# Optimization experiments

Hardware: AMD Instinct MI355X
Metric: run time of the kernel (lower is better)

Reference implementation:

```python
import jax, jax.numpy as jnp
import numpy as np

EPS = 1e-6
H, KV, HD = 16, 4, 64      # q heads, kv heads, head dim
BLK = 32                   # dllm_block_length (block-diffusion attention)
TOPK = 2                   # experts per token

def rmsnorm(x, w):
    return x * jax.lax.rsqrt(jnp.mean(x * x, axis=-1, keepdims=True) + EPS) * w

def rotate_half(x):
    x1, x2 = jnp.split(x, 2, axis=-1)
    return jnp.concatenate([-x2, x1], axis=-1)

def setup_inputs() -> dict:
    key = jax.random.key(0)
    ks = jax.random.split(key, 12)
    B, S, D = 1, 2048, 1024
    E, I = 8, 1024
    s = 0.02
    pos = jnp.arange(S, dtype=jnp.float32)
    inv_freq = 1.0 / (10000.0 ** (jnp.arange(0, HD, 2, dtype=jnp.float32) / HD))
    emb = jnp.concatenate([jnp.outer(pos, inv_freq)] * 2, axis=-1)  # [S, HD]
    return {
        'hidden_states': jax.random.normal(ks[0], (B, S, D), jnp.float32),
        'cos': jnp.cos(emb), 'sin': jnp.sin(emb),
        'w_qkv': jax.random.normal(ks[1], (D, (H + 2 * KV) * HD), jnp.float32) * s,
        'w_o': jax.random.normal(ks[2], (H * HD, D), jnp.float32) * s,
        'q_norm_w': jnp.ones((HD,), jnp.float32),
        'k_norm_w': jnp.ones((HD,), jnp.float32),
        'in_ln_w': jnp.ones((D,), jnp.float32),
        'post_ln_w': jnp.ones((D,), jnp.float32),
        'router_w': jax.random.normal(ks[3], (D, E), jnp.float32) * s,
        'w_gate': jax.random.normal(ks[4], (E, D, I), jnp.float32) * s,
        'w_up': jax.random.normal(ks[5], (E, D, I), jnp.float32) * s,
        'w_down': jax.random.normal(ks[6], (E, I, D), jnp.float32) * s,
        'ws_gate': jax.random.normal(ks[7], (D, I), jnp.float32) * s,
        'ws_up': jax.random.normal(ks[8], (D, I), jnp.float32) * s,
        'ws_down': jax.random.normal(ks[9], (I, D), jnp.float32) * s,
    }

def reference(hidden_states, cos, sin, w_qkv, w_o, q_norm_w, k_norm_w, in_ln_w,
              post_ln_w, router_w, w_gate, w_up, w_down, ws_gate, ws_up, ws_down):
    B, S, D = hidden_states.shape
    scale = HD ** -0.5
    # --- attention (pre-norm) ---
    h = rmsnorm(hidden_states, in_ln_w)
    qkv = h @ w_qkv
    q, k, v = jnp.split(qkv, [H * HD, (H + KV) * HD], axis=-1)
    q = q.reshape(B, S, H, HD); k = k.reshape(B, S, KV, HD); v = v.reshape(B, S, KV, HD)
    q = rmsnorm(q, q_norm_w); k = rmsnorm(k, k_norm_w)   # qk-norm per head
    c = cos[None, :, None, :]; sn = sin[None, :, None, :]
    q = q * c + rotate_half(q) * sn
    k = k * c + rotate_half(k) * sn
    rep = H // KV
    k = jnp.repeat(k, rep, axis=2); v = jnp.repeat(v, rep, axis=2)  # GQA expand
    scores = jnp.einsum('bqhd,bkhd->bhqk', q, k) * scale
    blk = jnp.arange(S) // BLK
    mask = blk[:, None] >= blk[None, :]   # block-causal: full attn inside block
    scores = jnp.where(mask[None, None], scores, jnp.float32(-1e30))
    p = jax.nn.softmax(scores, axis=-1)
    attn = jnp.einsum('bhqk,bkhd->bqhd', p, v).reshape(B, S, H * HD)
    x = hidden_states + attn @ w_o
    # --- MoE FFN (pre-norm) ---
    h2 = rmsnorm(x, post_ln_w)
    t = h2.reshape(B * S, D)
    logits = t.astype(jnp.float32) @ router_w.astype(jnp.float32)  # fp32 router
    probs = jax.nn.softmax(logits, axis=-1)
    topv, topi = jax.lax.top_k(probs, TOPK)
    topv = topv / jnp.sum(topv, axis=-1, keepdims=True)            # norm_topk_prob
    E = router_w.shape[1]
    w_tok = jnp.zeros((t.shape[0], E), jnp.float32).at[
        jnp.arange(t.shape[0])[:, None], topi].set(topv).astype(t.dtype)
    g = jnp.einsum('td,edi->tei', t, w_gate)
    u = jnp.einsum('td,edi->tei', t, w_up)
    eo = jnp.einsum('tei,eid->ted', jax.nn.silu(g) * u, w_down)
    moe = jnp.einsum('te,ted->td', w_tok, eo)
    shared = (jax.nn.silu(t @ ws_gate) * (t @ ws_up)) @ ws_down
    return x + (moe + shared).reshape(B, S, D)
```

## Files before the change

### kernel.cpp

```cpp
#include <hip/hip_runtime.h>
#include <hip/hip_bf16.h>
#include <math.h>

#define S 2048
#define D 1024
#define NH 16
#define NKV 4
#define HD 64
#define QKV_N 1536
#define NE 8
#define NI 1024
#define EPS 1e-6f

typedef __bf16 bf16_t;
typedef __bf16 __attribute__((may_alias)) abf16;
typedef __attribute__((ext_vector_type(8))) __bf16 bf16x8;
typedef __attribute__((ext_vector_type(4))) float f32x4;
union I4B8 { int4 i; bf16x8 v; bf16_t e[8]; };

__device__ __forceinline__ void gll16(const void* g, void* l) {
  __builtin_amdgcn_global_load_lds(
      (const __attribute__((address_space(1))) void*)g,
      (__attribute__((address_space(3))) void*)l, 16, 0, 0);
}


__global__ void rmsnorm_kernel(const float* __restrict__ in, const float* __restrict__ w,
                               float* __restrict__ out32, __hip_bfloat16* __restrict__ out16) {
  int t = blockIdx.x;
  int tid = threadIdx.x;
  const float* row = in + (size_t)t * D;
  float v[4];
  float ss = 0.f;
#pragma unroll
  for (int i = 0; i < 4; ++i) {
    v[i] = row[tid + i * 256];
    ss += v[i] * v[i];
  }
#pragma unroll
  for (int off = 32; off; off >>= 1) ss += __shfl_xor(ss, off);
  __shared__ float wsum[4];
  int wave = tid >> 6;
  if ((tid & 63) == 0) wsum[wave] = ss;
  __syncthreads();
  float tot = wsum[0] + wsum[1] + wsum[2] + wsum[3];
  float r = rsqrtf(tot / (float)D + EPS);
#pragma unroll
  for (int i = 0; i < 4; ++i) {
    int d = tid + i * 256;
    float val = v[i] * r * w[d];
    if (out32) out32[(size_t)t * D + d] = val;
    if (out16) out16[(size_t)t * D + d] = __float2bfloat16(val);
  }
}

__global__ void rmsnorm_router_kernel(const float* __restrict__ in, const float* __restrict__ w,
                                      const float* __restrict__ rw,
                                      __hip_bfloat16* __restrict__ out16,
                                      int* __restrict__ topk_e, float* __restrict__ topk_w) {
  int t = blockIdx.x;
  int tid = threadIdx.x;
  const float* row = in + (size_t)t * D;
  float v[4];
  float ss = 0.f;
#pragma unroll
  for (int i = 0; i < 4; ++i) {
    v[i] = row[tid + i * 256];
    ss += v[i] * v[i];
  }
#pragma unroll
  for (int off = 32; off; off >>= 1) ss += __shfl_xor(ss, off);
  __shared__ float wsum[4];
  __shared__ float pl[4][NE];
  int wave = tid >> 6, lane = tid & 63;
  if (lane == 0) wsum[wave] = ss;
  __syncthreads();
  float tot = wsum[0] + wsum[1] + wsum[2] + wsum[3];
  float r = rsqrtf(tot / (float)D + EPS);
  float p[NE] = {};
#pragma unroll
  for (int i = 0; i < 4; ++i) {
    int d = tid + i * 256;
    float val = v[i] * r * w[d];
    out16[(size_t)t * D + d] = __float2bfloat16(val);
    const float* rwd = rw + (size_t)d * NE;
#pragma unroll
    for (int e = 0; e < NE; ++e) p[e] += val * rwd[e];
  }
#pragma unroll
  for (int off = 32; off; off >>= 1)
#pragma unroll
    for (int e = 0; e < NE; ++e) p[e] += __shfl_xor(p[e], off);
  if (lane == 0)
#pragma unroll
    for (int e = 0; e < NE; ++e) pl[wave][e] = p[e];
  __syncthreads();
  if (tid == 0) {
    float q[NE];
#pragma unroll
    for (int e = 0; e < NE; ++e) q[e] = pl[0][e] + pl[1][e] + pl[2][e] + pl[3][e];
    float mx = q[0];
#pragma unroll
    for (int e = 1; e < NE; ++e) mx = fmaxf(mx, q[e]);
    float ex[NE];
#pragma unroll
    for (int e = 0; e < NE; ++e) ex[e] = __expf(q[e] - mx);
    int e0 = 0;
#pragma unroll
    for (int e = 1; e < NE; ++e) if (ex[e] > ex[e0]) e0 = e;
    int e1 = (e0 == 0) ? 1 : 0;
#pragma unroll
    for (int e = 0; e < NE; ++e) if (e != e0 && ex[e] > ex[e1]) e1 = e;
    float w0 = ex[e0] / (ex[e0] + ex[e1]);
    float w1 = ex[e1] / (ex[e0] + ex[e1]);
    topk_e[2 * t] = e0;  topk_e[2 * t + 1] = e1;
    topk_w[2 * t] = w0;  topk_w[2 * t + 1] = w1;
  }
}

__global__ void transpose_all_kernel(
    const float* __restrict__ w_qkv, const float* __restrict__ w_o,
    const float* __restrict__ w_gate, const float* __restrict__ w_up,
    const float* __restrict__ w_down, const float* __restrict__ ws_gate,
    const float* __restrict__ ws_up, const float* __restrict__ ws_down,
    __hip_bfloat16* wqkvT, __hip_bfloat16* woT, __hip_bfloat16* wgT,
    __hip_bfloat16* wuT, __hip_bfloat16* wdT, __hip_bfloat16* wsgT,
    __hip_bfloat16* wsuT, __hip_bfloat16* wsdT,
    const float* __restrict__ hidden, const float* __restrict__ in_ln,
    __hip_bfloat16* __restrict__ hb_out) {
  int z = blockIdx.z;
  int tid = threadIdx.x;
  if (z == 29) {
    __shared__ float wsum[4];
    int base = ((int)blockIdx.y * 24 + (int)blockIdx.x) * 6;
    int wave = tid >> 6;
#pragma unroll
    for (int jj = 0; jj < 6; ++jj) {
      int t = base + jj;
      if (t < S) {
        const float* row = hidden + (size_t)t * D;
        float v[4];
        float ss = 0.f;
#pragma unroll
        for (int i = 0; i < 4; ++i) {
          v[i] = row[tid + i * 256];
          ss += v[i] * v[i];
        }
#pragma unroll
        for (int off = 32; off; off >>= 1) ss += __shfl_xor(ss, off);
        if ((tid & 63) == 0) wsum[wave] = ss;
        __syncthreads();
        float tot = wsum[0] + wsum[1] + wsum[2] + wsum[3];
        float r = rsqrtf(tot / (float)D + EPS);
#pragma unroll
        for (int i = 0; i < 4; ++i) {
          int d = tid + i * 256;
          hb_out[(size_t)t * D + d] = __float2bfloat16(v[i] * r * in_ln[d]);
        }
      }
      __syncthreads();
    }
    return;
  }
  __shared__ __align__(16) bf16_t tile[64][72];
  const float* W; __hip_bfloat16* WT; int Kd, Nd;
  if (z == 0)       { W = w_qkv;  WT = wqkvT; Kd = D;  Nd = QKV_N; }
  else if (z == 1)  { W = w_o;    WT = woT;   Kd = D;  Nd = D; }
  else if (z < 10)  { int e = z - 2;  W = w_gate + (size_t)e * D * NI; WT = wgT + (size_t)e * D * NI; Kd = D;  Nd = NI; }
  else if (z < 18)  { int e = z - 10; W = w_up   + (size_t)e * D * NI; WT = wuT + (size_t)e * D * NI; Kd = D;  Nd = NI; }
  else if (z < 26)  { int e = z - 18; W = w_down + (size_t)e * NI * D; WT = wdT + (size_t)e * NI * D; Kd = NI; Nd = D; }
  else if (z == 26) { W = ws_gate; WT = wsgT; Kd = D;  Nd = NI; }
  else if (z == 27) { W = ws_up;   WT = wsuT; Kd = D;  Nd = NI; }
  else              { W = ws_down; WT = wsdT; Kd = NI; Nd = D; }
  int n0 = blockIdx.x * 64, k0 = blockIdx.y * 64;
  if (n0 >= Nd || k0 >= Kd) return;
  int rk = tid >> 4;
  int rc = (tid & 15) * 4;
#pragma unroll
  for (int it = 0; it < 4; ++it) {
    int k = it * 16 + rk;
    float4 v = *(const float4*)(W + (size_t)(k0 + k) * Nd + n0 + rc);
    union { bf16_t e[4]; int2 q; } pk4;
    pk4.e[0] = (bf16_t)v.x; pk4.e[1] = (bf16_t)v.y;
    pk4.e[2] = (bf16_t)v.z; pk4.e[3] = (bf16_t)v.w;
    *(int2*)&tile[k][rc] = pk4.q;
  }
  __syncthreads();
  int n = tid >> 2;
  int kc = (tid & 3) * 16;
  union { bf16_t e[16]; int4 q[2]; } pk;
#pragma unroll
  for (int j = 0; j < 16; ++j) pk.e[j] = tile[kc + j][n];
  int4* outp = (int4*)(WT + (size_t)(n0 + n) * Kd + k0 + kc);
  outp[0] = pk.q[0];
  outp[1] = pk.q[1];
}

__global__ __launch_bounds__(256) void mgemm_kernel(
    const __hip_bfloat16* __restrict__ A, const __hip_bfloat16* __restrict__ BT,
    const float* __restrict__ Cadd, float* __restrict__ C,
    int M, int N, int K,
    const int* __restrict__ counts, const int* __restrict__ offsets,
    const int* __restrict__ tok, int a_comp,
    const __hip_bfloat16* __restrict__ As2, const __hip_bfloat16* __restrict__ BTs2,
    float* __restrict__ Cs2) {
  __shared__ __align__(16) bf16_t Asd[2][128 * 32];
  __shared__ __align__(16) bf16_t Bsd[2][128 * 32];
  __shared__ int rowmap[128];
  int e = blockIdx.z;
  bool sh = (counts != nullptr) && (e == NE);
  int cnt = sh ? M : (counts ? counts[e] : M);
  int bm = blockIdx.y * 128;
  if (bm >= cnt) return;
  int bn = blockIdx.x * 128;
  int obase = sh ? 0 : (offsets ? offsets[e] : 0);
  const bf16_t* Ab = sh ? (const bf16_t*)As2 : (const bf16_t*)A;
  const bf16_t* BTe = sh ? (const bf16_t*)BTs2 : ((const bf16_t*)BT + (size_t)e * N * K);
  float* Cp = sh ? Cs2 : C;
  const int* toke = (!sh && tok) ? tok + e * S : nullptr;
  int acompe = sh ? 0 : a_comp;
  int tid = threadIdx.x;
  if (tid < 128) {
    int gp = bm + tid;
    int cp = gp < cnt ? gp : cnt - 1;
    rowmap[tid] = toke ? toke[cp] : (acompe ? obase + cp : cp);
  }
  __syncthreads();
  int wave = tid >> 6, lane = tid & 63;
  int quad = lane >> 4, l16 = lane & 15;
  int wm = wave >> 1, wn = wave & 1;
  int srow = tid >> 2, scol = (tid & 3) * 8;
  size_t aoff0 = (size_t)rowmap[srow] * K + scol;
  size_t aoff1 = (size_t)rowmap[64 + srow] * K + scol;
  size_t boff0 = (size_t)(bn + srow) * K + scol;
  size_t boff1 = (size_t)(bn + 64 + srow) * K + scol;
  f32x4 acc[4][4];
#pragma unroll
  for (int i = 0; i < 4; ++i)
#pragma unroll
    for (int j = 0; j < 4; ++j) acc[i][j] = (f32x4){0.f, 0.f, 0.f, 0.f};

  {
    char* AsB = (char*)Asd[0] + wave * 1024;
    char* BsB = (char*)Bsd[0] + wave * 1024;
    gll16(Ab + aoff0, AsB);
    gll16(Ab + aoff1, AsB + 4096);
    gll16(BTe + boff0, BsB);
    gll16(BTe + boff1, BsB + 4096);
  }
  for (int k0 = 0; k0 < K; k0 += 32) {
    int cur = (k0 >> 5) & 1;
    __syncthreads();
    if (k0 + 32 < K) {
      char* AsB = (char*)Asd[cur ^ 1] + wave * 1024;
      char* BsB = (char*)Bsd[cur ^ 1] + wave * 1024;
      gll16(Ab + aoff0 + k0 + 32, AsB);
      gll16(Ab + aoff1 + k0 + 32, AsB + 4096);
      gll16(BTe + boff0 + k0 + 32, BsB);
      gll16(BTe + boff1 + k0 + 32, BsB + 4096);
    }
    I4B8 af[4], bfr[4];
#pragma unroll
    for (int i = 0; i < 4; ++i)
      af[i].i = *(const int4*)(Asd[cur] + (wm * 64 + i * 16 + l16) * 32 + quad * 8);
#pragma unroll
    for (int j = 0; j < 4; ++j)
      bfr[j].i = *(const int4*)(Bsd[cur] + (wn * 64 + j * 16 + l16) * 32 + quad * 8);
#pragma unroll
    for (int i = 0; i < 4; ++i)
#pragma unroll
      for (int j = 0; j < 4; ++j)
        acc[i][j] = __builtin_amdgcn_mfma_f32_16x16x32_bf16(af[i].v, bfr[j].v, acc[i][j], 0, 0, 0);
  }
#pragma unroll
  for (int i = 0; i < 4; ++i) {
#pragma unroll
    for (int r = 0; r < 4; ++r) {
      int trow = wm * 64 + i * 16 + quad * 4 + r;
      int gp = bm + trow;
      if (gp < cnt) {
        size_t rowb = (size_t)(obase + gp) * N;
#pragma unroll
        for (int j = 0; j < 4; ++j) {
          int col = bn + wn * 64 + j * 16 + l16;
          size_t idx = rowb + col;
          Cp[idx] = acc[i][j][r] + (Cadd ? Cadd[idx] : 0.f);
        }
      }
    }
  }
}

__global__ __launch_bounds__(256) void mgemm_gu_kernel(
    const __hip_bfloat16* __restrict__ A, const __hip_bfloat16* __restrict__ BTg,
    const __hip_bfloat16* __restrict__ BTu, __hip_bfloat16* __restrict__ act,
    int M, int N, int K,
    const int* __restrict__ counts, const int* __restrict__ offsets,
    const int* __restrict__ tok,
    const __hip_bfloat16* __restrict__ BTgs, const __hip_bfloat16* __restrict__ BTus,
    __hip_bfloat16* __restrict__ acts) {
  __shared__ __align__(16) bf16_t Asd[2][128 * 32];
  __shared__ __align__(16) bf16_t Bgd[2][64 * 32];
  __shared__ __align__(16) bf16_t Bud[2][64 * 32];
  __shared__ int rowmap[128];
  int e = blockIdx.z;
  bool sh = (counts != nullptr) && (e == NE);
  int cnt = sh ? M : (counts ? counts[e] : M);
  int bm = blockIdx.y * 128;
  if (bm >= cnt) return;
  int bn = blockIdx.x * 64;
  const bf16_t* Ab = (const bf16_t*)A;
  const bf16_t* Bg = sh ? (const bf16_t*)BTgs : ((const bf16_t*)BTg + (size_t)e * N * K);
  const bf16_t* Bu = sh ? (const bf16_t*)BTus : ((const bf16_t*)BTu + (size_t)e * N * K);
  bf16_t* outp = sh ? (bf16_t*)acts : (bf16_t*)act;
  int obase = sh ? 0 : (offsets ? offsets[e] : 0);
  const int* toke = (!sh && tok) ? tok + e * S : nullptr;
  int tid = threadIdx.x;
  if (tid < 128) {
    int gp = bm + tid;
    int cp = gp < cnt ? gp : cnt - 1;
    rowmap[tid] = toke ? toke[cp] : cp;
  }
  __syncthreads();
  int wave = tid >> 6, lane = tid & 63;
  int quad = lane >> 4, l16 = lane & 15;
  int wm = wave >> 1, wn = wave & 1;
  int srow = tid >> 2, scol = (tid & 3) * 8;
  size_t aoff0 = (size_t)rowmap[srow] * K + scol;
  size_t aoff1 = (size_t)rowmap[64 + srow] * K + scol;
  size_t boff = (size_t)(bn + srow) * K + scol;
  f32x4 accg[4][2], accu[4][2];
#pragma unroll
  for (int i = 0; i < 4; ++i)
#pragma unroll
    for (int j = 0; j < 2; ++j) {
      accg[i][j] = (f32x4){0.f, 0.f, 0.f, 0.f};
      accu[i][j] = (f32x4){0.f, 0.f, 0.f, 0.f};
    }
  {
    char* AsB = (char*)Asd[0] + wave * 1024;
    gll16(Ab + aoff0, AsB);
    gll16(Ab + aoff1, AsB + 4096);
    gll16(Bg + boff, (char*)Bgd[0] + wave * 1024);
    gll16(Bu + boff, (char*)Bud[0] + wave * 1024);
  }
  for (int k0 = 0; k0 < K; k0 += 32) {
    int cur = (k0 >> 5) & 1;
    __syncthreads();
    if (k0 + 32 < K) {
      char* AsB = (char*)Asd[cur ^ 1] + wave * 1024;
      gll16(Ab + aoff0 + k0 + 32, AsB);
      gll16(Ab + aoff1 + k0 + 32, AsB + 4096);
      gll16(Bg + boff + k0 + 32, (char*)Bgd[cur ^ 1] + wave * 1024);
      gll16(Bu + boff + k0 + 32, (char*)Bud[cur ^ 1] + wave * 1024);
    }
    I4B8 af[4], bg[2], bu[2];
#pragma unroll
    for (int i = 0; i < 4; ++i)
      af[i].i = *(const int4*)(Asd[cur] + (wm * 64 + i * 16 + l16) * 32 + quad * 8);
#pragma unroll
    for (int j = 0; j < 2; ++j) {
      bg[j].i = *(const int4*)(Bgd[cur] + (wn * 32 + j * 16 + l16) * 32 + quad * 8);
      bu[j].i = *(const int4*)(Bud[cur] + (wn * 32 + j * 16 + l16) * 32 + quad * 8);
    }
#pragma unroll
    for (int i = 0; i < 4; ++i)
#pragma unroll
      for (int j = 0; j < 2; ++j) {
        accg[i][j] = __builtin_amdgcn_mfma_f32_16x16x32_bf16(af[i].v, bg[j].v, accg[i][j], 0, 0, 0);
        accu[i][j] = __builtin_amdgcn_mfma_f32_16x16x32_bf16(af[i].v, bu[j].v, accu[i][j], 0, 0, 0);
      }
  }
#pragma unroll
  for (int i = 0; i < 4; ++i) {
#pragma unroll
    for (int r = 0; r < 4; ++r) {
      int trow = wm * 64 + i * 16 + quad * 4 + r;
      int gp = bm + trow;
      if (gp < cnt) {
        size_t rowb = (size_t)(obase + gp) * N;
#pragma unroll
        for (int j = 0; j < 2; ++j) {
          int col = bn + wn * 32 + j * 16 + l16;
          float g = accg[i][j][r], uu = accu[i][j][r];
          float sg = g / (1.f + __expf(-g));
          outp[rowb + col] = __float2bfloat16(sg * uu);
        }
      }
    }
  }
}

__global__ void qkv_post_kernel(const float* __restrict__ qkv,
                                const float* __restrict__ qw, const float* __restrict__ kw,
                                const float* __restrict__ cosb, const float* __restrict__ sinb,
                                __hip_bfloat16* __restrict__ qout,
                                __hip_bfloat16* __restrict__ kout,
                                __hip_bfloat16* __restrict__ vT) {
  __shared__ float tile[32][33];
  if (blockIdx.y == 5) {
    int bx = blockIdx.x;
    if (bx < 512) {
      int t0 = (bx & 63) * 32;
      int c0 = (bx >> 6) * 32;
      int tx = threadIdx.x & 31, ty = threadIdx.x >> 5;
#pragma unroll
      for (int i = 0; i < 4; ++i)
        tile[ty + i * 8][tx] = qkv[(size_t)(t0 + ty + i * 8) * QKV_N + (NH + NKV) * HD + c0 + tx];
      __syncthreads();
#pragma unroll
      for (int i = 0; i < 4; ++i)
        vT[(size_t)(c0 + ty + i * 8) * S + t0 + tx] = __float2bfloat16(tile[tx][ty + i * 8]);
    }
    return;
  }
  int t = blockIdx.x;
  int u = blockIdx.y * 4 + (threadIdx.x >> 6);
  int lane = threadIdx.x & 63;
  bool isq = (u < NH);
  int h = isq ? u : (u - NH);
  size_t src = (size_t)t * QKV_N + (isq ? (h * HD) : (NH * HD + h * HD)) + lane;
  float xv = qkv[src];
  float ss = xv * xv;
#pragma unroll
  for (int off = 32; off; off >>= 1) ss += __shfl_xor(ss, off);
  float r = rsqrtf(ss * (1.f / 64.f) + EPS);
  float xn = xv * r * (isq ? qw[lane] : kw[lane]);
  float other = __shfl_xor(xn, 32);
  float rot = (lane < 32) ? -other : other;
  float res = xn * cosb[t * 64 + lane] + rot * sinb[t * 64 + lane];
  if (isq) qout[(size_t)t * (NH * HD) + h * HD + lane] = __float2bfloat16(res * 0.125f);
  else     kout[(size_t)t * (NKV * HD) + h * HD + lane] = __float2bfloat16(res);
}

__global__ __launch_bounds__(256) void attn_kernel(
    const __hip_bfloat16* __restrict__ qg, const __hip_bfloat16* __restrict__ kg,
    const __hip_bfloat16* __restrict__ vT,
    float* __restrict__ opart0, float* __restrict__ opart1,
    float* __restrict__ mpart, float* __restrict__ lpart) {
  int qt = (int)(gridDim.x - 1) - (int)blockIdx.x;
  int kvh = blockIdx.y;
  int z = blockIdx.z;
  int tid = threadIdx.x;
  int wave = tid >> 6, lane = tid & 63;
  int quad = lane >> 4, l16 = lane & 15;
  int h = kvh * 4 + wave;

  float* opz = z ? opart1 : opart0;
  float* mp = mpart + (size_t)z * S * NH;
  float* lp = lpart + (size_t)z * S * NH;

  int nb = (qt >> 1) + 1;
  int nt = (nb + 1) >> 1;
  bool halfm = (nb & 1) != 0;
  int h0 = nt >> 1;
  int lo = z ? h0 : 0;
  int hi = z ? nt : h0;

  if (lo >= hi) {
    int row = qt * 16 + (tid >> 4);
    float* od = opz + (size_t)row * (NH * HD) + kvh * 256 + (tid & 15) * 16;
    int4 zz = {0, 0, 0, 0};
#pragma unroll
    for (int i = 0; i < 4; ++i) *(int4*)(od + i * 4) = zz;
    if (tid < 64) {
      int rr = qt * 16 + (tid >> 2), hh = kvh * 4 + (tid & 3);
      mp[(size_t)rr * NH + hh] = -1e30f;
      lp[(size_t)rr * NH + hh] = 0.f;
    }
    return;
  }

  __shared__ __align__(16) int KsI[64 * 36];
  __shared__ __align__(16) int VTI[64 * 36];
  __shared__ __align__(16) int PsI[4][16 * 36];

  I4B8 qf[2];
#pragma unroll
  for (int ch = 0; ch < 2; ++ch)
    qf[ch].i = *(const int4*)((const abf16*)qg +
        (size_t)(qt * 16 + l16) * (NH * HD) + h * HD + ch * 32 + quad * 8);

  I4B8 ones;
  ones.i = (int4){0x3F803F80, 0x3F803F80, 0x3F803F80, 0x3F803F80};

  float m_r[4];
  f32x4 o[4], o4;
#pragma unroll
  for (int r = 0; r < 4; ++r) m_r[r] = -1e30f;
#pragma unroll
  for (int sub = 0; sub < 4; ++sub) o[sub] = (f32x4){0.f, 0.f, 0.f, 0.f};
  o4 = (f32x4){0.f, 0.f, 0.f, 0.f};

  int sp = tid >> 3, sc = tid & 7;
  const abf16* kb = (const abf16*)kg;
  const abf16* vb = (const abf16*)vT;

  int4 rk0 = *(const int4*)(kb + (size_t)(lo * 64 + sp) * (NKV * HD) + kvh * HD + sc * 8);
  int4 rk1 = *(const int4*)(kb + (size_t)(lo * 64 + 32 + sp) * (NKV * HD) + kvh * HD + sc * 8);
  int4 rv0 = *(const int4*)(vb + (size_t)(kvh * HD + sp) * S + lo * 64 + sc * 8);
  int4 rv1 = *(const int4*)(vb + (size_t)(kvh * HD + 32 + sp) * S + lo * 64 + sc * 8);

  for (int kc = lo; kc < hi; ++kc) {
    *(int4*)&KsI[sp * 36 + sc * 4] = rk0;
    *(int4*)&KsI[(sp + 32) * 36 + sc * 4] = rk1;
    *(int4*)&VTI[sp * 36 + sc * 4] = rv0;
    *(int4*)&VTI[(sp + 32) * 36 + sc * 4] = rv1;
    __syncthreads();

    if (kc + 1 < hi) {
      rk0 = *(const int4*)(kb + (size_t)((kc + 1) * 64 + sp) * (NKV * HD) + kvh * HD + sc * 8);
      rk1 = *(const int4*)(kb + (size_t)((kc + 1) * 64 + 32 + sp) * (NKV * HD) + kvh * HD + sc * 8);
      rv0 = *(const int4*)(vb + (size_t)(kvh * HD + sp) * S + (kc + 1) * 64 + sc * 8);
      rv1 = *(const int4*)(vb + (size_t)(kvh * HD + 32 + sp) * S + (kc + 1) * 64 + sc * 8);
    }

    f32x4 s[4];
#pragma unroll
    for (int sub = 0; sub < 4; ++sub) s[sub] = (f32x4){0.f, 0.f, 0.f, 0.f};
    __builtin_amdgcn_s_setprio(1);
#pragma unroll
    for (int sub = 0; sub < 4; ++sub)
#pragma unroll
      for (int ch = 0; ch < 2; ++ch) {
        I4B8 ku;
        ku.i = *(const int4*)&KsI[(sub * 16 + l16) * 36 + ch * 16 + quad * 4];
        s[sub] = __builtin_amdgcn_mfma_f32_16x16x32_bf16(qf[ch].v, ku.v, s[sub], 0, 0, 0);
      }
    __builtin_amdgcn_s_setprio(0);
    if (halfm && kc == nt - 1) {
#pragma unroll
      for (int r = 0; r < 4; ++r) { s[2][r] = -1e30f; s[3][r] = -1e30f; }
    }

    abf16* pw = (abf16*)PsI[wave];
#pragma unroll
    for (int r = 0; r < 4; ++r) {
      float v = fmaxf(fmaxf(s[0][r], s[1][r]), fmaxf(s[2][r], s[3][r]));
#pragma unroll
      for (int off = 1; off < 16; off <<= 1) v = fmaxf(v, __shfl_xor(v, off));
      float mx = fmaxf(m_r[r], v);
      float al = __expf(m_r[r] - mx);
      m_r[r] = mx;
      float p0 = __expf(s[0][r] - mx);
      float p1 = __expf(s[1][r] - mx);
      float p2 = __expf(s[2][r] - mx);
      float p3 = __expf(s[3][r] - mx);
      int prow = quad * 4 + r;
      pw[prow * 72 + l16]      = (bf16_t)p0;
      pw[prow * 72 + 16 + l16] = (bf16_t)p1;
      pw[prow * 72 + 32 + l16] = (bf16_t)p2;
      pw[prow * 72 + 48 + l16] = (bf16_t)p3;
      o4[r] *= al;
#pragma unroll
      for (int sub = 0; sub < 4; ++sub) o[sub][r] *= al;
    }

    I4B8 pu[2];
#pragma unroll
    for (int ch = 0; ch < 2; ++ch)
      pu[ch].i = *(const int4*)&PsI[wave][l16 * 36 + ch * 16 + quad * 4];
    __builtin_amdgcn_s_setprio(1);
#pragma unroll
    for (int sub = 0; sub < 4; ++sub)
#pragma unroll
      for (int ch = 0; ch < 2; ++ch) {
        I4B8 vf;
        vf.i = *(const int4*)&VTI[(sub * 16 + l16) * 36 + ch * 16 + quad * 4];
        o[sub] = __builtin_amdgcn_mfma_f32_16x16x32_bf16(pu[ch].v, vf.v, o[sub], 0, 0, 0);
      }
#pragma unroll
    for (int ch = 0; ch < 2; ++ch)
      o4 = __builtin_amdgcn_mfma_f32_16x16x32_bf16(pu[ch].v, ones.v, o4, 0, 0, 0);
    __builtin_amdgcn_s_setprio(0);
    __syncthreads();
  }

#pragma unroll
  for (int r = 0; r < 4; ++r) {
    int row = qt * 16 + quad * 4 + r;
    float* od = opz + (size_t)row * (NH * HD) + h * HD;
#pragma unroll
    for (int sub = 0; sub < 4; ++sub)
      od[sub * 16 + l16] = o[sub][r];
    if (l16 == 0) {
      mp[(size_t)row * NH + h] = m_r[r];
      lp[(size_t)row * NH + h] = o4[r];
    }
  }
}

__global__ void attn_merge_kernel(const float* __restrict__ opart0,
                                  const float* __restrict__ opart1,
                                  const float* __restrict__ mpart,
                                  const float* __restrict__ lpart,
                                  __hip_bfloat16* __restrict__ attn) {
  int row = blockIdx.x;
  int tid = threadIdx.x;
#pragma unroll
  for (int i = 0; i < 4; ++i) {
    int c = tid + i * 256;
    int h = c >> 6;
    float m0 = mpart[(size_t)row * NH + h];
    float m1 = mpart[(size_t)(S + row) * NH + h];
    float l0 = lpart[(size_t)row * NH + h];
    float l1 = lpart[(size_t)(S + row) * NH + h];
    float M = fmaxf(m0, m1);
    float a0 = __expf(m0 - M), a1 = __expf(m1 - M);
    float l = l0 * a0 + l1 * a1;
    float v = (opart0[(size_t)row * (NH * HD) + c] * a0 +
               opart1[(size_t)row * (NH * HD) + c] * a1) / l;
    attn[(size_t)row * (NH * HD) + c] = __float2bfloat16(v);
  }
}

__global__ __launch_bounds__(1024) void router_place_kernel(
    const int* __restrict__ topk_e, int* __restrict__ counts, int* __restrict__ offsets,
    int* __restrict__ tok_list, int* __restrict__ topk_pos) {
  __shared__ int lcnt[NE];
  int tid = threadIdx.x;
  int lane = tid & 63;
  if (tid < NE) lcnt[tid] = 0;
  __syncthreads();
#pragma unroll
  for (int r = 0; r < 2; ++r) {
    int t = r * 1024 + tid;
#pragma unroll
    for (int s = 0; s < 2; ++s) {
      int e = topk_e[2 * t + s];
      int pos = 0;
#pragma unroll
      for (int x = 0; x < NE; ++x) {
        unsigned long long mask = __ballot(e == x);
        if (mask) {
          int leader = __ffsll((unsigned long long)mask) - 1;
          int cnt = __popcll(mask);
          int base = 0;
          if (lane == leader) base = atomicAdd(&lcnt[x], cnt);
          base = __shfl(base, leader);
          if (e == x)
            pos = base + __popcll(mask & ((1ull << lane) - 1ull));
        }
      }
      topk_pos[2 * t + s] = pos;
      tok_list[e * S + pos] = t;
    }
  }
  __syncthreads();
  if (tid == 0) {
    int acc = 0;
    for (int e = 0; e < NE; ++e) { offsets[e] = acc; counts[e] = lcnt[e]; acc += lcnt[e]; }
  }
}

__global__ void final_kernel(const float* __restrict__ x, const float* __restrict__ sout,
                             const float* __restrict__ eo,
                             const int* __restrict__ topk_e, const int* __restrict__ topk_pos,
                             const float* __restrict__ topk_w, const int* __restrict__ offsets,
                             float* __restrict__ out) {
  int t = blockIdx.x;
  int tid = threadIdx.x;
  int e0 = topk_e[2 * t], e1 = topk_e[2 * t + 1];
  size_t r0 = (size_t)offsets[e0] + topk_pos[2 * t];
  size_t r1 = (size_t)offsets[e1] + topk_pos[2 * t + 1];
  float w0 = topk_w[2 * t], w1 = topk_w[2 * t + 1];
#pragma unroll
  for (int i = 0; i < 4; ++i) {
    int d = tid + i * 256;
    size_t idx = (size_t)t * D + d;
    out[idx] = x[idx] + sout[idx] + w0 * eo[r0 * D + d] + w1 * eo[r1 * D + d];
  }
}

extern "C" void kernel_launch(void* const* d_in, const int* in_sizes, int n_in,
                              void* d_out, int out_size, void* d_ws, size_t ws_size,
                              hipStream_t stream) {
  const float* hidden  = (const float*)d_in[0];
  const float* cosb    = (const float*)d_in[1];
  const float* sinb    = (const float*)d_in[2];
  const float* w_qkv   = (const float*)d_in[3];
  const float* w_o     = (const float*)d_in[4];
  const float* q_norm  = (const float*)d_in[5];
  const float* k_norm  = (const float*)d_in[6];
  const float* in_ln   = (const float*)d_in[7];
  const float* post_ln = (const float*)d_in[8];
  const float* router_w= (const float*)d_in[9];
  const float* w_gate  = (const float*)d_in[10];
  const float* w_up    = (const float*)d_in[11];
  const float* w_down  = (const float*)d_in[12];
  const float* ws_gate = (const float*)d_in[13];
  const float* ws_up   = (const float*)d_in[14];
  const float* ws_down = (const float*)d_in[15];
  float* out = (float*)d_out;
  float* ws = (float*)d_ws;

  typedef __hip_bfloat16 hbf;
  hbf* wqkvT = (hbf*)(ws);
  hbf* woT   = (hbf*)(ws +  768 * 1024);
  hbf* wgT   = (hbf*)(ws + 1280 * 1024);
  hbf* wuT   = (hbf*)(ws + 5376 * 1024);
  hbf* wdT   = (hbf*)(ws + 9472 * 1024);
  hbf* wsgT  = (hbf*)(ws + 13568 * 1024);
  hbf* wsuT  = (hbf*)(ws + 14080 * 1024);
  hbf* wsdT  = (hbf*)(ws + 14592 * 1024);
  hbf*   hb      = (hbf*)(ws + 15104 * 1024);
  float* qkv     = ws + 16128 * 1024;
  hbf*   qbB     = (hbf*)(ws + 19200 * 1024);
  hbf*   kbB     = (hbf*)(ws + 20224 * 1024);
  hbf*   vTb     = (hbf*)(ws + 20480 * 1024);
  hbf*   attnb16 = (hbf*)(ws + 20736 * 1024);
  float* x       = ws + 22784 * 1024;
  hbf*   h2b     = (hbf*)(ws + 26880 * 1024);
  hbf*   act     = (hbf*)(ws + 16128 * 1024);
  float* eo      = ws + 18176 * 1024;
  hbf*   sact    = (hbf*)(ws + 27904 * 1024);
  float* sout    = ws + 28928 * 1024;
  float* mpart   = ws + 15104 * 1024;
  float* lpart   = mpart + 2 * S * NH;
  float* opart0  = ws + 16128 * 1024;
  float* opart1  = ws + 22784 * 1024;
  int* counts   = (int*)(ws + 30976 * 1024);
  int* offsets  = counts + NE;
  int* tok_list = offsets + NE;
  int* topk_e   = tok_list + NE * S;
  int* topk_pos = topk_e + 2 * S;
  float* topk_w = (float*)(topk_pos + 2 * S);

  dim3 b256(256);
  transpose_all_kernel<<<dim3(24, 16, 30), b256, 0, stream>>>(
      w_qkv, w_o, w_gate, w_up, w_down, ws_gate, ws_up, ws_down,
      wqkvT, woT, wgT, wuT, wdT, wsgT, wsuT, wsdT,
      hidden, in_ln, hb);
  mgemm_kernel<<<dim3(QKV_N/128, S/128, 1), b256, 0, stream>>>(hb, wqkvT, nullptr, qkv,
      S, QKV_N, D, nullptr, nullptr, nullptr, 0, nullptr, nullptr, nullptr);
  qkv_post_kernel<<<dim3(S, 6), b256, 0, stream>>>(qkv, q_norm, k_norm, cosb, sinb, qbB, kbB, vTb);
  attn_kernel<<<dim3(S/16, NKV, 2), b256, 0, stream>>>(qbB, kbB, vTb,
      opart0, opart1, mpart, lpart);
  attn_merge_kernel<<<S, b256, 0, stream>>>(opart0, opart1, mpart, lpart, attnb16);
  mgemm_kernel<<<dim3(D/128, S/128, 1), b256, 0, stream>>>(attnb16, woT, hidden, x,
      S, D, D, nullptr, nullptr, nullptr, 0, nullptr, nullptr, nullptr);
  rmsnorm_router_kernel<<<S, b256, 0, stream>>>(x, post_ln, router_w, h2b, topk_e, topk_w);
  router_place_kernel<<<1, 1024, 0, stream>>>(topk_e, counts, offsets, tok_list, topk_pos);
  mgemm_gu_kernel<<<dim3(NI/64, S/128, NE + 1), b256, 0, stream>>>(h2b, wgT, wuT, act,
      S, NI, D, counts, offsets, tok_list, wsgT, wsuT, sact);
  mgemm_kernel<<<dim3(D/128, S/128, NE + 1), b256, 0, stream>>>(act, wdT, nullptr, eo,
      S, D, NI, counts, offsets, nullptr, 1, sact, wsdT, sout);
  final_kernel<<<S, b256, 0, stream>>>(x, sout, eo, topk_e, topk_pos, topk_w, offsets, out);
}
```

Before: 423.0 us.

## Split attention KV range four ways and use 128x64 tiles for dense GEMMs

Raises the attention split-K factor from 2 to 4 partitions, with a four-way log-sum-exp merge, so more workgroups share the long causal rows. The QKV and output-projection GEMMs move to a new 128x64-tile kernel, which doubles the workgroup count for these small-N dense GEMMs and gives better CU occupancy on the large GPU. The costs are more partial-output traffic in fp32 and extra merge reads. Workspace regions are reused for the two new partial buffers, which relies on those regions being dead at that point.

```diff
diff --git a/kernel.cpp b/kernel.cpp
--- a/kernel.cpp
+++ b/kernel.cpp
@@ -24,35 +24,6 @@
       (__attribute__((address_space(3))) void*)l, 16, 0, 0);
 }
 
-
-__global__ void rmsnorm_kernel(const float* __restrict__ in, const float* __restrict__ w,
-                               float* __restrict__ out32, __hip_bfloat16* __restrict__ out16) {
-  int t = blockIdx.x;
-  int tid = threadIdx.x;
-  const float* row = in + (size_t)t * D;
-  float v[4];
-  float ss = 0.f;
-#pragma unroll
-  for (int i = 0; i < 4; ++i) {
-    v[i] = row[tid + i * 256];
-    ss += v[i] * v[i];
-  }
-#pragma unroll
-  for (int off = 32; off; off >>= 1) ss += __shfl_xor(ss, off);
-  __shared__ float wsum[4];
-  int wave = tid >> 6;
-  if ((tid & 63) == 0) wsum[wave] = ss;
-  __syncthreads();
-  float tot = wsum[0] + wsum[1] + wsum[2] + wsum[3];
-  float r = rsqrtf(tot / (float)D + EPS);
-#pragma unroll
-  for (int i = 0; i < 4; ++i) {
-    int d = tid + i * 256;
-    float val = v[i] * r * w[d];
-    if (out32) out32[(size_t)t * D + d] = val;
-    if (out16) out16[(size_t)t * D + d] = __float2bfloat16(val);
-  }
-}
 
 __global__ void rmsnorm_router_kernel(const float* __restrict__ in, const float* __restrict__ w,
                                       const float* __restrict__ rw,
@@ -286,6 +257,73 @@
           size_t idx = rowb + col;
           Cp[idx] = acc[i][j][r] + (Cadd ? Cadd[idx] : 0.f);
         }
+      }
+    }
+  }
+}
+
+__global__ __launch_bounds__(256) void mgemm_n64_kernel(
+    const __hip_bfloat16* __restrict__ A, const __hip_bfloat16* __restrict__ BT,
+    const float* __restrict__ Cadd, float* __restrict__ C,
+    int M, int N, int K) {
+  __shared__ __align__(16) bf16_t Asd[2][128 * 32];
+  __shared__ __align__(16) bf16_t Bsd[2][64 * 32];
+  int bm = blockIdx.y * 128;
+  int bn = blockIdx.x * 64;
+  int tid = threadIdx.x;
+  int wave = tid >> 6, lane = tid & 63;
+  int quad = lane >> 4, l16 = lane & 15;
+  int wm = wave >> 1, wn = wave & 1;
+  int srow = tid >> 2, scol = (tid & 3) * 8;
+  size_t aoff0 = (size_t)(bm + srow) * K + scol;
+  size_t aoff1 = (size_t)(bm + 64 + srow) * K + scol;
+  size_t boff = (size_t)(bn + srow) * K + scol;
+  const bf16_t* Ab = (const bf16_t*)A;
+  const bf16_t* Bb = (const bf16_t*)BT;
+  f32x4 acc[4][2];
+#pragma unroll
+  for (int i = 0; i < 4; ++i)
+#pragma unroll
+    for (int j = 0; j < 2; ++j) acc[i][j] = (f32x4){0.f, 0.f, 0.f, 0.f};
+  {
+    char* AsB = (char*)Asd[0] + wave * 1024;
+    gll16(Ab + aoff0, AsB);
+    gll16(Ab + aoff1, AsB + 4096);
+    gll16(Bb + boff, (char*)Bsd[0] + wave * 1024);
+  }
+  for (int k0 = 0; k0 < K; k0 += 32) {
+    int cur = (k0 >> 5) & 1;
+    __syncthreads();
+    if (k0 + 32 < K) {
+      char* AsB = (char*)Asd[cur ^ 1] + wave * 1024;
+      gll16(Ab + aoff0 + k0 + 32, AsB);
+      gll16(Ab + aoff1 + k0 + 32, AsB + 4096);
+      gll16(Bb + boff + k0 + 32, (char*)Bsd[cur ^ 1] + wave * 1024);
+    }
+    I4B8 af[4], bf[2];
+#pragma unroll
+    for (int i = 0; i < 4; ++i)
+      af[i].i = *(const int4*)(Asd[cur] + (wm * 64 + i * 16 + l16) * 32 + quad * 8);
+#pragma unroll
+    for (int j = 0; j < 2; ++j)
+      bf[j].i = *(const int4*)(Bsd[cur] + (wn * 32 + j * 16 + l16) * 32 + quad * 8);
+#pragma unroll
+    for (int i = 0; i < 4; ++i)
+#pragma unroll
+      for (int j = 0; j < 2; ++j)
+        acc[i][j] = __builtin_amdgcn_mfma_f32_16x16x32_bf16(af[i].v, bf[j].v, acc[i][j], 0, 0, 0);
+  }
+#pragma unroll
+  for (int i = 0; i < 4; ++i) {
+#pragma unroll
+    for (int r = 0; r < 4; ++r) {
+      int gp = bm + wm * 64 + i * 16 + quad * 4 + r;
+      size_t rowb = (size_t)gp * N;
+#pragma unroll
+      for (int j = 0; j < 2; ++j) {
+        int col = bn + wn * 32 + j * 16 + l16;
+        size_t idx = rowb + col;
+        C[idx] = acc[i][j][r] + (Cadd ? Cadd[idx] : 0.f);
       }
     }
   }
@@ -436,7 +474,8 @@
 __global__ __launch_bounds__(256) void attn_kernel(
     const __hip_bfloat16* __restrict__ qg, const __hip_bfloat16* __restrict__ kg,
     const __hip_bfloat16* __restrict__ vT,
-    float* __restrict__ opart0, float* __restrict__ opart1,
+    float* __restrict__ op0, float* __restrict__ op1,
+    float* __restrict__ op2, float* __restrict__ op3,
     float* __restrict__ mpart, float* __restrict__ lpart) {
   int qt = (int)(gridDim.x - 1) - (int)blockIdx.x;
   int kvh = blockIdx.y;
@@ -446,16 +485,15 @@
   int quad = lane >> 4, l16 = lane & 15;
   int h = kvh * 4 + wave;
 
-  float* opz = z ? opart1 : opart0;
+  float* opz = (z == 0) ? op0 : (z == 1) ? op1 : (z == 2) ? op2 : op3;
   float* mp = mpart + (size_t)z * S * NH;
   float* lp = lpart + (size_t)z * S * NH;
 
   int nb = (qt >> 1) + 1;
   int nt = (nb + 1) >> 1;
   bool halfm = (nb & 1) != 0;
-  int h0 = nt >> 1;
-  int lo = z ? h0 : 0;
-  int hi = z ? nt : h0;
+  int lo = (nt * z) >> 2;
+  int hi = (nt * (z + 1)) >> 2;
 
   if (lo >= hi) {
     int row = qt * 16 + (tid >> 4);
@@ -590,8 +628,10 @@
   }
 }
 
-__global__ void attn_merge_kernel(const float* __restrict__ opart0,
-                                  const float* __restrict__ opart1,
+__global__ void attn_merge_kernel(const float* __restrict__ op0,
+                                  const float* __restrict__ op1,
+                                  const float* __restrict__ op2,
+                                  const float* __restrict__ op3,
                                   const float* __restrict__ mpart,
                                   const float* __restrict__ lpart,
                                   __hip_bfloat16* __restrict__ attn) {
@@ -603,14 +643,19 @@
     int h = c >> 6;
     float m0 = mpart[(size_t)row * NH + h];
     float m1 = mpart[(size_t)(S + row) * NH + h];
+    float m2 = mpart[(size_t)(2 * S + row) * NH + h];
+    float m3 = mpart[(size_t)(3 * S + row) * NH + h];
     float l0 = lpart[(size_t)row * NH + h];
     float l1 = lpart[(size_t)(S + row) * NH + h];
-    float M = fmaxf(m0, m1);
+    float l2 = lpart[(size_t)(2 * S + row) * NH + h];
+    float l3 = lpart[(size_t)(3 * S + row) * NH + h];
+    float M = fmaxf(fmaxf(m0, m1), fmaxf(m2, m3));
     float a0 = __expf(m0 - M), a1 = __expf(m1 - M);
-    float l = l0 * a0 + l1 * a1;
-    float v = (opart0[(size_t)row * (NH * HD) + c] * a0 +
-               opart1[(size_t)row * (NH * HD) + c] * a1) / l;
-    attn[(size_t)row * (NH * HD) + c] = __float2bfloat16(v);
+    float a2 = __expf(m2 - M), a3 = __expf(m3 - M);
+    float l = l0 * a0 + l1 * a1 + l2 * a2 + l3 * a3;
+    size_t idx = (size_t)row * (NH * HD) + c;
+    float v = (op0[idx] * a0 + op1[idx] * a1 + op2[idx] * a2 + op3[idx] * a3) / l;
+    attn[idx] = __float2bfloat16(v);
   }
 }
 
@@ -716,9 +761,11 @@
   hbf*   sact    = (hbf*)(ws + 27904 * 1024);
   float* sout    = ws + 28928 * 1024;
   float* mpart   = ws + 15104 * 1024;
-  float* lpart   = mpart + 2 * S * NH;
+  float* lpart   = mpart + 4 * S * NH;
   float* opart0  = ws + 16128 * 1024;
   float* opart1  = ws + 22784 * 1024;
+  float* opart2  = ws + 28928 * 1024;
+  float* opart3  = ws + 26880 * 1024;
   int* counts   = (int*)(ws + 30976 * 1024);
   int* offsets  = counts + NE;
   int* tok_list = offsets + NE;
@@ -731,14 +778,15 @@
       w_qkv, w_o, w_gate, w_up, w_down, ws_gate, ws_up, ws_down,
       wqkvT, woT, wgT, wuT, wdT, wsgT, wsuT, wsdT,
       hidden, in_ln, hb);
-  mgemm_kernel<<<dim3(QKV_N/128, S/128, 1), b256, 0, stream>>>(hb, wqkvT, nullptr, qkv,
-      S, QKV_N, D, nullptr, nullptr, nullptr, 0, nullptr, nullptr, nullptr);
+  mgemm_n64_kernel<<<dim3(QKV_N/64, S/128), b256, 0, stream>>>(hb, wqkvT, nullptr, qkv,
+      S, QKV_N, D);
   qkv_post_kernel<<<dim3(S, 6), b256, 0, stream>>>(qkv, q_norm, k_norm, cosb, sinb, qbB, kbB, vTb);
-  attn_kernel<<<dim3(S/16, NKV, 2), b256, 0, stream>>>(qbB, kbB, vTb,
-      opart0, opart1, mpart, lpart);
-  attn_merge_kernel<<<S, b256, 0, stream>>>(opart0, opart1, mpart, lpart, attnb16);
-  mgemm_kernel<<<dim3(D/128, S/128, 1), b256, 0, stream>>>(attnb16, woT, hidden, x,
-      S, D, D, nullptr, nullptr, nullptr, 0, nullptr, nullptr, nullptr);
+  attn_kernel<<<dim3(S/16, NKV, 4), b256, 0, stream>>>(qbB, kbB, vTb,
+      opart0, opart1, opart2, opart3, mpart, lpart);
+  attn_merge_kernel<<<S, b256, 0, stream>>>(opart0, opart1, opart2, opart3,
+      mpart, lpart, attnb16);
+  mgemm_n64_kernel<<<dim3(D/64, S/128), b256, 0, stream>>>(attnb16, woT, hidden, x,
+      S, D, D);
   rmsnorm_router_kernel<<<S, b256, 0, stream>>>(x, post_ln, router_w, h2b, topk_e, topk_w);
   router_place_kernel<<<1, 1024, 0, stream>>>(topk_e, counts, offsets, tok_list, topk_pos);
   mgemm_gu_kernel<<<dim3(NI/64, S/128, NE + 1), b256, 0, stream>>>(h2b, wgT, wuT, act,
```

Result: faster. 396.1 us (-6.4%).
